# Kernel optimization log

Hardware: AMD Instinct MI355X
Metric: run time of the kernel (lower is better)

Reference implementation:

```python
import jax, jax.numpy as jnp
import numpy as np

D_MODEL = 1024
D_STATE = 16
D_CONV = 4
EXPAND = 2
D_INNER = EXPAND * D_MODEL
B, L = 4, 2048


def setup_inputs() -> dict:
    key = jax.random.key(0)
    ks = jax.random.split(key, 8)
    s = 0.02
    x = jax.random.normal(ks[0], (B, L, D_MODEL), jnp.float32)
    W_in = jax.random.normal(ks[1], (D_MODEL, 2 * D_INNER), jnp.float32) * s
    conv_w = jax.random.normal(ks[2], (D_INNER, D_CONV), jnp.float32) * 0.1
    conv_b = jnp.zeros((D_INNER,), jnp.float32)
    W_x = jax.random.normal(ks[3], (D_INNER, 1 + 2 * D_STATE), jnp.float32) * s
    w_dt = jax.random.normal(ks[4], (D_INNER,), jnp.float32) * 0.1
    b_dt = jnp.zeros((D_INNER,), jnp.float32)
    # A_log initialized exactly as in the torch module: log of [1..d_state] per channel
    A_log = jnp.log(jnp.tile(jnp.arange(1, D_STATE + 1, dtype=jnp.float32), (D_INNER, 1)))
    D = jnp.ones((D_INNER,), jnp.float32)
    W_out = jax.random.normal(ks[5], (D_INNER, D_MODEL), jnp.float32) * s
    return {"x": x, "W_in": W_in, "conv_w": conv_w, "conv_b": conv_b,
            "W_x": W_x, "w_dt": w_dt, "b_dt": b_dt, "A_log": A_log,
            "D": D, "W_out": W_out}


def _mamba_forward(x, W_in, conv_w, conv_b, W_x, w_dt, b_dt, A_log, D, W_out):
    Bb, Ll, _ = x.shape
    # input projection -> x branch and gate z
    xz = x @ W_in                                  # [B, L, 2*d_inner]
    xc, z = jnp.split(xz, 2, axis=-1)
    # depthwise causal conv1d (left-pad d_conv-1, cross-correlation like torch Conv1d)
    xp = jnp.pad(xc, ((0, 0), (D_CONV - 1, 0), (0, 0)))
    xconv = conv_b
    for k in range(D_CONV):                        # tiny fixed kernel loop
        xconv = xconv + xp[:, k:k + Ll, :] * conv_w[:, k]
    xs = jax.nn.silu(xconv)                        # [B, L, d_inner]
    # selective SSM parameters
    A = -jnp.exp(A_log)                            # [d_inner, d_state]
    x_dbl = xs @ W_x                               # [B, L, 1+2N]
    d_raw = x_dbl[..., :1]
    Bp = x_dbl[..., 1:1 + D_STATE]                 # [B, L, N]
    Cp = x_dbl[..., 1 + D_STATE:]                  # [B, L, N]
    delta = jax.nn.softplus(d_raw * w_dt + b_dt)   # [B, L, d_inner]

    def step(h, inp):
        dt, b, c, xt = inp                         # [B,d_inner],[B,N],[B,N],[B,d_inner]
        At = jnp.exp(dt[..., None] * A)            # [B, d_inner, N]
        h = At * h + (dt * xt)[..., None] * b[:, None, :]
        y = jnp.einsum('bdn,bn->bd', h, c)
        return h, y

    h0 = jnp.zeros((Bb, D_INNER, D_STATE), x.dtype)
    seq = (jnp.swapaxes(delta, 0, 1), jnp.swapaxes(Bp, 0, 1),
           jnp.swapaxes(Cp, 0, 1), jnp.swapaxes(xs, 0, 1))
    _, ys = jax.lax.scan(step, h0, seq)            # ys: [L, B, d_inner]
    y = jnp.swapaxes(ys, 0, 1) + xs * D
    y = y * jax.nn.silu(z)
    return y @ W_out                               # [B, L, d_model]


def reference(x, W_in, conv_w, conv_b, W_x, w_dt, b_dt, A_log, D, W_out):
    return _mamba_forward(x, W_in, conv_w, conv_b, W_x, w_dt, b_dt, A_log, D, W_out)
```

## Files before the change

### kernel.cpp

```cpp
#include <hip/hip_runtime.h>
#include <hip/hip_bf16.h>


typedef __attribute__((ext_vector_type(8))) short short8;
typedef __attribute__((ext_vector_type(8))) __bf16 bf16x8;
typedef __attribute__((ext_vector_type(4))) float f32x4;

__device__ inline short bf16_bits(float f) {
  __hip_bfloat16 h = __float2bfloat16(f);
  return *(short*)&h;
}

__global__ void transpose_cast_kernel(const float* __restrict__ in,
                                      __hip_bfloat16* __restrict__ out, int R, int C) {
  __shared__ float tile[32][33];
  int tx = threadIdx.x, ty = threadIdx.y;
  int x = blockIdx.x * 32 + tx;
  int y0 = blockIdx.y * 32;
#pragma unroll
  for (int j = 0; j < 32; j += 8)
    tile[ty + j][tx] = in[(size_t)(y0 + ty + j) * C + x];
  __syncthreads();
  int x2 = y0 + tx;
  int y2 = blockIdx.x * 32;
#pragma unroll
  for (int j = 0; j < 32; j += 8)
    out[(size_t)(y2 + ty + j) * R + x2] = __float2bfloat16(tile[tx][ty + j]);
}

__global__ void wx_pad_kernel(const float* __restrict__ wx,
                              __hip_bfloat16* __restrict__ out) {
  int i = blockIdx.x * 256 + threadIdx.x;
  int j = i >> 11;
  int k = i & 2047;
  float v = (j < 33) ? wx[k * 33 + j] : 0.f;
  out[i] = __float2bfloat16(v);
}

__global__ __launch_bounds__(256) void gemm_bt(
    const void* __restrict__ Aptr, const __hip_bfloat16* __restrict__ BTbf,
    void* __restrict__ C0, void* __restrict__ C1,
    int M, int N, int K, int a_f32, int mode) {
  __shared__ __align__(16) short As[128 * 32];
  __shared__ __align__(16) short Bs[128 * 32];
  int tid = threadIdx.x;
  int bm = blockIdx.y, bn = blockIdx.x;
  int lane = tid & 63, w = tid >> 6;
  int wm = w >> 1, wn = w & 1;
  int l16 = lane & 15, quad = lane >> 4;

  int Kslice = K / (int)gridDim.z;
  int kbeg = (int)blockIdx.z * Kslice;

  f32x4 acc[4][4] = {};

  const short* Ag16 = (const short*)Aptr + (size_t)bm * 128 * K + kbeg;
  const float* Ag32 = (const float*)Aptr + (size_t)bm * 128 * K + kbeg;
  const short* Bg = (const short*)BTbf + (size_t)bn * 128 * K + kbeg;

  int r0 = tid >> 2;
  int c0 = (tid & 3) * 8;

  for (int k0 = 0; k0 < Kslice; k0 += 32) {
    short8 a0, a1;
    if (a_f32) {
      const float* p0 = &Ag32[(size_t)r0 * K + k0 + c0];
      const float* p1 = &Ag32[(size_t)(r0 + 64) * K + k0 + c0];
      float4 u0 = *(const float4*)p0, v0 = *(const float4*)(p0 + 4);
      float4 u1 = *(const float4*)p1, v1 = *(const float4*)(p1 + 4);
      a0[0] = bf16_bits(u0.x); a0[1] = bf16_bits(u0.y);
      a0[2] = bf16_bits(u0.z); a0[3] = bf16_bits(u0.w);
      a0[4] = bf16_bits(v0.x); a0[5] = bf16_bits(v0.y);
      a0[6] = bf16_bits(v0.z); a0[7] = bf16_bits(v0.w);
      a1[0] = bf16_bits(u1.x); a1[1] = bf16_bits(u1.y);
      a1[2] = bf16_bits(u1.z); a1[3] = bf16_bits(u1.w);
      a1[4] = bf16_bits(v1.x); a1[5] = bf16_bits(v1.y);
      a1[6] = bf16_bits(v1.z); a1[7] = bf16_bits(v1.w);
    } else {
      a0 = *(const short8*)&Ag16[(size_t)r0 * K + k0 + c0];
      a1 = *(const short8*)&Ag16[(size_t)(r0 + 64) * K + k0 + c0];
    }
    short8 b0 = *(const short8*)&Bg[(size_t)r0 * K + k0 + c0];
    short8 b1 = *(const short8*)&Bg[(size_t)(r0 + 64) * K + k0 + c0];
    __syncthreads();
    *(short8*)&As[r0 * 32 + c0] = a0;
    *(short8*)&As[(r0 + 64) * 32 + c0] = a1;
    *(short8*)&Bs[r0 * 32 + c0] = b0;
    *(short8*)&Bs[(r0 + 64) * 32 + c0] = b1;
    __syncthreads();

    bf16x8 af[4], bfr[4];
#pragma unroll
    for (int mt = 0; mt < 4; ++mt)
      af[mt] = *(bf16x8*)&As[(wm * 64 + mt * 16 + l16) * 32 + quad * 8];
#pragma unroll
    for (int nt = 0; nt < 4; ++nt)
      bfr[nt] = *(bf16x8*)&Bs[(wn * 64 + nt * 16 + l16) * 32 + quad * 8];
#pragma unroll
    for (int mt = 0; mt < 4; ++mt)
#pragma unroll
      for (int nt = 0; nt < 4; ++nt)
        acc[mt][nt] = __builtin_amdgcn_mfma_f32_16x16x32_bf16(af[mt], bfr[nt],
                                                              acc[mt][nt], 0, 0, 0);
  }

#pragma unroll
  for (int mt = 0; mt < 4; ++mt) {
#pragma unroll
    for (int nt = 0; nt < 4; ++nt) {
#pragma unroll
      for (int i = 0; i < 4; ++i) {
        int row = bm * 128 + wm * 64 + mt * 16 + quad * 4 + i;
        int col = bn * 128 + wn * 64 + nt * 16 + l16;
        float v = acc[mt][nt][i];
        if (mode == 0) {
          ((float*)C0)[(size_t)row * N + col] = v;
        } else if (mode == 2) {
          atomicAdd(&((float*)C0)[(size_t)row * N + col], v);
        } else {
          if (col < 2048) {
            ((__hip_bfloat16*)C0)[(size_t)row * 2048 + col] = __float2bfloat16(v);
          } else {
            float s = v / (1.f + __expf(-v));
            ((__hip_bfloat16*)C1)[(size_t)row * 2048 + (col - 2048)] =
                __float2bfloat16(s);
          }
        }
      }
    }
  }
}

__global__ void conv_silu_kernel(const __hip_bfloat16* __restrict__ xc,
                                 const float* __restrict__ conv_w,
                                 const float* __restrict__ conv_b,
                                 __hip_bfloat16* __restrict__ xs_bf) {
  int i = blockIdx.x * 256 + threadIdx.x;
  int d = i & 2047;
  int row = i >> 11;
  int l = row & 2047;
  float acc = conv_b[d];
#pragma unroll
  for (int k = 0; k < 4; ++k) {
    int lj = l - 3 + k;
    if (lj >= 0)
      acc += __bfloat162float(xc[(size_t)(row - 3 + k) * 2048 + d]) * conv_w[d * 4 + k];
  }
  float s = acc / (1.f + __expf(-acc));
  xs_bf[i] = __float2bfloat16(s);
}

template <int FINAL>
__global__ __launch_bounds__(256) void scan_seg(
    const float* __restrict__ xdbl, const __hip_bfloat16* __restrict__ xs,
    const __hip_bfloat16* __restrict__ sz,
    const float* __restrict__ w_dt, const float* __restrict__ b_dt,
    const float* __restrict__ Dvec, const float* __restrict__ hio,
    float* __restrict__ hloc, float* __restrict__ sdtA,
    __hip_bfloat16* __restrict__ y_bf) {
  const int t = threadIdx.x;
  const int b = blockIdx.y, seg = blockIdx.z;
  const int d = blockIdx.x * 256 + t;
  const int brow0 = b * 2048 + seg * 128;

  __shared__ __align__(16) float s_xd[16][36];
  __shared__ ushort s_xs[16][256];
  __shared__ ushort s_sz[16][256];

  float h[16];
  const float wdt = w_dt[d], bdt = b_dt[d];
  float Dd = 0.f, sdt = 0.f;
  const size_t hbase = ((size_t)(seg * 4 + b) * 2048 + d) * 16;
  if (FINAL) {
    Dd = Dvec[d];
#pragma unroll
    for (int n = 0; n < 16; n += 4) *(float4*)&h[n] = *(const float4*)&hio[hbase + n];
  } else {
#pragma unroll
    for (int n = 0; n < 16; ++n) h[n] = 0.f;
  }

  for (int c = 0; c < 8; ++c) {
    const int r0 = brow0 + c * 16;
    __syncthreads();
    if (t < 144) {
      int row = t / 9, q = t - row * 9;
      *(float4*)&s_xd[row][q * 4] =
          *(const float4*)&xdbl[(size_t)(r0 + row) * 128 + q * 4];
    }
#pragma unroll
    for (int r = 0; r < 16; ++r) {
      s_xs[r][t] = ((const ushort*)xs)[(size_t)(r0 + r) * 2048 + d];
      if (FINAL) s_sz[r][t] = ((const ushort*)sz)[(size_t)(r0 + r) * 2048 + d];
    }
    __syncthreads();
#pragma unroll
    for (int r = 0; r < 16; ++r) {
      float pre = __builtin_fmaf(s_xd[r][0], wdt, bdt);
      float ex = __expf(pre);
      float dtv = (pre > 20.f) ? pre : __logf(1.f + ex);
      float E = __expf(-dtv);
      float p2 = E * E, p4 = p2 * p2, p8 = p4 * p4;
      float at[16];
      at[0] = E;        at[1] = p2;       at[2] = p2 * E;   at[3] = p4;
      at[4] = p4 * E;   at[5] = p4 * p2;  at[6] = p4 * at[2]; at[7] = p8;
      at[8] = p8 * E;   at[9] = p8 * p2;  at[10] = p8 * at[2]; at[11] = p8 * p4;
      at[12] = p8 * at[4]; at[13] = p8 * at[5]; at[14] = p8 * at[6]; at[15] = p8 * p8;
      ushort ux = s_xs[r][t];
      float xsv = __bfloat162float(*(__hip_bfloat16*)&ux);
      float w = dtv * xsv;
      float y = 0.f;
#pragma unroll
      for (int n = 0; n < 16; ++n) {
        h[n] = __builtin_fmaf(at[n], h[n], w * s_xd[r][1 + n]);
        if (FINAL) y = __builtin_fmaf(h[n], s_xd[r][17 + n], y);
      }
      if (FINAL) {
        ushort uz = s_sz[r][t];
        float szv = __bfloat162float(*(__hip_bfloat16*)&uz);
        float yv = (y + xsv * Dd) * szv;
        y_bf[(size_t)(r0 + r) * 2048 + d] = __float2bfloat16(yv);
      } else {
        sdt += dtv;
      }
    }
  }
  if (!FINAL) {
#pragma unroll
    for (int n = 0; n < 16; n += 4) *(float4*)&hloc[hbase + n] = *(const float4*)&h[n];
    sdtA[(seg * 4 + b) * 2048 + d] = sdt;
  }
}

__global__ void scan_mid(float* __restrict__ hio, const float* __restrict__ sdtA,
                         const float* __restrict__ A_log) {
  int gid = blockIdx.x * 256 + threadIdx.x;
  int n = gid & 15, dd = (gid >> 4) & 2047;
  float A = -__expf(A_log[dd * 16 + n]);
  float h = 0.f;
#pragma unroll
  for (int s = 0; s < 16; ++s) {
    float v = hio[s * 131072 + gid];
    float P = __expf(A * sdtA[s * 8192 + (gid >> 4)]);
    float nh = __builtin_fmaf(P, h, v);
    hio[s * 131072 + gid] = h;
    h = nh;
  }
}

extern "C" void kernel_launch(void* const* d_in, const int* in_sizes, int n_in,
                              void* d_out, int out_size, void* d_ws, size_t ws_size,
                              hipStream_t stream) {
  const float* x      = (const float*)d_in[0];
  const float* W_in   = (const float*)d_in[1];
  const float* conv_w = (const float*)d_in[2];
  const float* conv_b = (const float*)d_in[3];
  const float* W_x    = (const float*)d_in[4];
  const float* w_dt   = (const float*)d_in[5];
  const float* b_dt   = (const float*)d_in[6];
  const float* A_log  = (const float*)d_in[7];
  const float* Dv     = (const float*)d_in[8];
  const float* W_out  = (const float*)d_in[9];
  float* out = (float*)d_out;

  char* ws = (char*)d_ws;
  const size_t MB = 1ull << 20;
  __hip_bfloat16* xc_bf = (__hip_bfloat16*)(ws + 0);
  __hip_bfloat16* y_bf  = (__hip_bfloat16*)(ws + 0);
  __hip_bfloat16* sz_bf = (__hip_bfloat16*)(ws + 32 * MB);
  __hip_bfloat16* xs_bf = (__hip_bfloat16*)(ws + 64 * MB);
  __hip_bfloat16* WinT  = (__hip_bfloat16*)(ws + 96 * MB);
  float*          hio   = (float*)(ws + 96 * MB);
  __hip_bfloat16* WoutT = (__hip_bfloat16*)(ws + 104 * MB);
  __hip_bfloat16* WxT   = (__hip_bfloat16*)(ws + 108 * MB);
  float*          sdtA  = (float*)(ws + 108 * MB);
  float*          xdbl  = (float*)(ws + 108 * MB + 512 * 1024);

  transpose_cast_kernel<<<dim3(128, 32), dim3(32, 8), 0, stream>>>(W_in, WinT, 1024, 4096);
  transpose_cast_kernel<<<dim3(32, 64), dim3(32, 8), 0, stream>>>(W_out, WoutT, 2048, 1024);
  wx_pad_kernel<<<1024, 256, 0, stream>>>(W_x, WxT);

  gemm_bt<<<dim3(32, 64), 256, 0, stream>>>(x, WinT, xc_bf, sz_bf, 8192, 4096, 1024, 1, 1);
  conv_silu_kernel<<<65536, 256, 0, stream>>>(xc_bf, conv_w, conv_b, xs_bf);
  hipMemsetAsync(xdbl, 0, 8192 * 128 * sizeof(float), stream);
  gemm_bt<<<dim3(1, 64, 4), 256, 0, stream>>>(xs_bf, WxT, xdbl, nullptr, 8192, 128, 2048, 0, 2);

  scan_seg<0><<<dim3(8, 4, 16), 256, 0, stream>>>(xdbl, xs_bf, nullptr, w_dt, b_dt,
                                                  nullptr, nullptr, hio, sdtA, nullptr);
  scan_mid<<<512, 256, 0, stream>>>(hio, sdtA, A_log);
  scan_seg<1><<<dim3(8, 4, 16), 256, 0, stream>>>(xdbl, xs_bf, sz_bf, w_dt, b_dt,
                                                  Dv, hio, nullptr, nullptr, y_bf);

  gemm_bt<<<dim3(8, 64), 256, 0, stream>>>(y_bf, WoutT, out, nullptr, 8192, 1024, 2048, 0, 0);
}
```

Before: 517.0 us.

## Use direct global-to-LDS loads in GEMM, pre-cast x, vectorize conv

```diff
diff --git a/kernel.cpp b/kernel.cpp
--- a/kernel.cpp
+++ b/kernel.cpp
@@ -5,10 +5,32 @@
 typedef __attribute__((ext_vector_type(8))) short short8;
 typedef __attribute__((ext_vector_type(8))) __bf16 bf16x8;
 typedef __attribute__((ext_vector_type(4))) float f32x4;
+typedef __attribute__((ext_vector_type(8))) unsigned short ushort8v;
+typedef __attribute__((ext_vector_type(4))) unsigned short ushort4v;
 
 __device__ inline short bf16_bits(float f) {
   __hip_bfloat16 h = __float2bfloat16(f);
   return *(short*)&h;
+}
+__device__ inline float bfbits2f(unsigned short u) {
+  return __uint_as_float(((unsigned)u) << 16);
+}
+
+#define GLL16(gp, lp)                                                        \
+  __builtin_amdgcn_global_load_lds(                                          \
+      (const __attribute__((address_space(1))) void*)(gp),                   \
+      (__attribute__((address_space(3))) void*)(lp), 16, 0, 0)
+
+__global__ void cast_bf16_kernel(const float* __restrict__ in,
+                                 unsigned short* __restrict__ out) {
+  int i = blockIdx.x * 256 + threadIdx.x;
+  float4 v = ((const float4*)in)[i];
+  ushort4v o;
+  o.x = (unsigned short)bf16_bits(v.x);
+  o.y = (unsigned short)bf16_bits(v.y);
+  o.z = (unsigned short)bf16_bits(v.z);
+  o.w = (unsigned short)bf16_bits(v.w);
+  *(ushort4v*)&out[4 * i] = o;
 }
 
 __global__ void transpose_cast_kernel(const float* __restrict__ in,
@@ -38,9 +60,9 @@
 }
 
 __global__ __launch_bounds__(256) void gemm_bt(
-    const void* __restrict__ Aptr, const __hip_bfloat16* __restrict__ BTbf,
+    const __hip_bfloat16* __restrict__ Abf, const __hip_bfloat16* __restrict__ BTbf,
     void* __restrict__ C0, void* __restrict__ C1,
-    int M, int N, int K, int a_f32, int mode) {
+    int M, int N, int K, int mode) {
   __shared__ __align__(16) short As[128 * 32];
   __shared__ __align__(16) short Bs[128 * 32];
   int tid = threadIdx.x;
@@ -54,39 +76,22 @@
 
   f32x4 acc[4][4] = {};
 
-  const short* Ag16 = (const short*)Aptr + (size_t)bm * 128 * K + kbeg;
-  const float* Ag32 = (const float*)Aptr + (size_t)bm * 128 * K + kbeg;
+  const short* Ag = (const short*)Abf + (size_t)bm * 128 * K + kbeg;
   const short* Bg = (const short*)BTbf + (size_t)bn * 128 * K + kbeg;
 
-  int r0 = tid >> 2;
-  int c0 = (tid & 3) * 8;
+  int srow = w * 16 + (lane >> 2);
+  int scol = (lane & 3) * 8;
+  const short* agp = &Ag[(size_t)srow * K + scol];
+  const short* bgp = &Bg[(size_t)srow * K + scol];
+  short* asl = &As[w * 512];
+  short* bsl = &Bs[w * 512];
 
   for (int k0 = 0; k0 < Kslice; k0 += 32) {
-    short8 a0, a1;
-    if (a_f32) {
-      const float* p0 = &Ag32[(size_t)r0 * K + k0 + c0];
-      const float* p1 = &Ag32[(size_t)(r0 + 64) * K + k0 + c0];
-      float4 u0 = *(const float4*)p0, v0 = *(const float4*)(p0 + 4);
-      float4 u1 = *(const float4*)p1, v1 = *(const float4*)(p1 + 4);
-      a0[0] = bf16_bits(u0.x); a0[1] = bf16_bits(u0.y);
-      a0[2] = bf16_bits(u0.z); a0[3] = bf16_bits(u0.w);
-      a0[4] = bf16_bits(v0.x); a0[5] = bf16_bits(v0.y);
-      a0[6] = bf16_bits(v0.z); a0[7] = bf16_bits(v0.w);
-      a1[0] = bf16_bits(u1.x); a1[1] = bf16_bits(u1.y);
-      a1[2] = bf16_bits(u1.z); a1[3] = bf16_bits(u1.w);
-      a1[4] = bf16_bits(v1.x); a1[5] = bf16_bits(v1.y);
-      a1[6] = bf16_bits(v1.z); a1[7] = bf16_bits(v1.w);
-    } else {
-      a0 = *(const short8*)&Ag16[(size_t)r0 * K + k0 + c0];
-      a1 = *(const short8*)&Ag16[(size_t)(r0 + 64) * K + k0 + c0];
-    }
-    short8 b0 = *(const short8*)&Bg[(size_t)r0 * K + k0 + c0];
-    short8 b1 = *(const short8*)&Bg[(size_t)(r0 + 64) * K + k0 + c0];
     __syncthreads();
-    *(short8*)&As[r0 * 32 + c0] = a0;
-    *(short8*)&As[(r0 + 64) * 32 + c0] = a1;
-    *(short8*)&Bs[r0 * 32 + c0] = b0;
-    *(short8*)&Bs[(r0 + 64) * 32 + c0] = b1;
+    GLL16(agp + k0, asl);
+    GLL16(agp + (size_t)64 * K + k0, asl + 64 * 32);
+    GLL16(bgp + k0, bsl);
+    GLL16(bgp + (size_t)64 * K + k0, bsl + 64 * 32);
     __syncthreads();
 
     bf16x8 af[4], bfr[4];
@@ -131,23 +136,44 @@
   }
 }
 
-__global__ void conv_silu_kernel(const __hip_bfloat16* __restrict__ xc,
+__global__ void conv_silu_kernel(const unsigned short* __restrict__ xc,
                                  const float* __restrict__ conv_w,
                                  const float* __restrict__ conv_b,
-                                 __hip_bfloat16* __restrict__ xs_bf) {
+                                 unsigned short* __restrict__ xs_bf) {
   int i = blockIdx.x * 256 + threadIdx.x;
-  int d = i & 2047;
-  int row = i >> 11;
+  int g = i & 255;
+  int row = i >> 8;
   int l = row & 2047;
-  float acc = conv_b[d];
+  int d = g * 8;
+
+  float4 cw[8];
+#pragma unroll
+  for (int j = 0; j < 8; ++j) cw[j] = ((const float4*)conv_w)[d + j];
+
+  float acc[8];
+  {
+    float4 b0 = ((const float4*)conv_b)[g * 2];
+    float4 b1 = ((const float4*)conv_b)[g * 2 + 1];
+    acc[0] = b0.x; acc[1] = b0.y; acc[2] = b0.z; acc[3] = b0.w;
+    acc[4] = b1.x; acc[5] = b1.y; acc[6] = b1.z; acc[7] = b1.w;
+  }
 #pragma unroll
   for (int k = 0; k < 4; ++k) {
-    int lj = l - 3 + k;
-    if (lj >= 0)
-      acc += __bfloat162float(xc[(size_t)(row - 3 + k) * 2048 + d]) * conv_w[d * 4 + k];
-  }
-  float s = acc / (1.f + __expf(-acc));
-  xs_bf[i] = __float2bfloat16(s);
+    if (l - 3 + k >= 0) {
+      ushort8v v = *(const ushort8v*)&xc[(size_t)(row - 3 + k) * 2048 + d];
+      const float* wk = (const float*)cw;
+#pragma unroll
+      for (int j = 0; j < 8; ++j)
+        acc[j] = __builtin_fmaf(bfbits2f(v[j]), wk[j * 4 + k], acc[j]);
+    }
+  }
+  ushort8v o;
+#pragma unroll
+  for (int j = 0; j < 8; ++j) {
+    float s = acc[j] / (1.f + __expf(-acc[j]));
+    o[j] = (unsigned short)bf16_bits(s);
+  }
+  *(ushort8v*)&xs_bf[(size_t)row * 2048 + d] = o;
 }
 
 template <int FINAL>
@@ -202,12 +228,11 @@
       float E = __expf(-dtv);
       float p2 = E * E, p4 = p2 * p2, p8 = p4 * p4;
       float at[16];
-      at[0] = E;        at[1] = p2;       at[2] = p2 * E;   at[3] = p4;
+      at[0] = E;        at[1] = p2;       at[2] = p2 * E;     at[3] = p4;
       at[4] = p4 * E;   at[5] = p4 * p2;  at[6] = p4 * at[2]; at[7] = p8;
       at[8] = p8 * E;   at[9] = p8 * p2;  at[10] = p8 * at[2]; at[11] = p8 * p4;
       at[12] = p8 * at[4]; at[13] = p8 * at[5]; at[14] = p8 * at[6]; at[15] = p8 * p8;
-      ushort ux = s_xs[r][t];
-      float xsv = __bfloat162float(*(__hip_bfloat16*)&ux);
+      float xsv = bfbits2f(s_xs[r][t]);
       float w = dtv * xsv;
       float y = 0.f;
 #pragma unroll
@@ -216,8 +241,7 @@
         if (FINAL) y = __builtin_fmaf(h[n], s_xd[r][17 + n], y);
       }
       if (FINAL) {
-        ushort uz = s_sz[r][t];
-        float szv = __bfloat162float(*(__hip_bfloat16*)&uz);
+        float szv = bfbits2f(s_sz[r][t]);
         float yv = (y + xsv * Dd) * szv;
         y_bf[(size_t)(r0 + r) * 2048 + d] = __float2bfloat16(yv);
       } else {
@@ -269,6 +293,7 @@
   __hip_bfloat16* y_bf  = (__hip_bfloat16*)(ws + 0);
   __hip_bfloat16* sz_bf = (__hip_bfloat16*)(ws + 32 * MB);
   __hip_bfloat16* xs_bf = (__hip_bfloat16*)(ws + 64 * MB);
+  __hip_bfloat16* x_bf  = (__hip_bfloat16*)(ws + 64 * MB);
   __hip_bfloat16* WinT  = (__hip_bfloat16*)(ws + 96 * MB);
   float*          hio   = (float*)(ws + 96 * MB);
   __hip_bfloat16* WoutT = (__hip_bfloat16*)(ws + 104 * MB);
@@ -276,14 +301,16 @@
   float*          sdtA  = (float*)(ws + 108 * MB);
   float*          xdbl  = (float*)(ws + 108 * MB + 512 * 1024);
 
+  cast_bf16_kernel<<<8192, 256, 0, stream>>>(x, (unsigned short*)x_bf);
   transpose_cast_kernel<<<dim3(128, 32), dim3(32, 8), 0, stream>>>(W_in, WinT, 1024, 4096);
   transpose_cast_kernel<<<dim3(32, 64), dim3(32, 8), 0, stream>>>(W_out, WoutT, 2048, 1024);
   wx_pad_kernel<<<1024, 256, 0, stream>>>(W_x, WxT);
 
-  gemm_bt<<<dim3(32, 64), 256, 0, stream>>>(x, WinT, xc_bf, sz_bf, 8192, 4096, 1024, 1, 1);
-  conv_silu_kernel<<<65536, 256, 0, stream>>>(xc_bf, conv_w, conv_b, xs_bf);
+  gemm_bt<<<dim3(32, 64), 256, 0, stream>>>(x_bf, WinT, xc_bf, sz_bf, 8192, 4096, 1024, 1);
+  conv_silu_kernel<<<8192, 256, 0, stream>>>((const unsigned short*)xc_bf, conv_w, conv_b,
+                                             (unsigned short*)xs_bf);
   hipMemsetAsync(xdbl, 0, 8192 * 128 * sizeof(float), stream);
-  gemm_bt<<<dim3(1, 64, 4), 256, 0, stream>>>(xs_bf, WxT, xdbl, nullptr, 8192, 128, 2048, 0, 2);
+  gemm_bt<<<dim3(1, 64, 4), 256, 0, stream>>>(xs_bf, WxT, xdbl, nullptr, 8192, 128, 2048, 2);
 
   scan_seg<0><<<dim3(8, 4, 16), 256, 0, stream>>>(xdbl, xs_bf, nullptr, w_dt, b_dt,
                                                   nullptr, nullptr, hio, sdtA, nullptr);
@@ -291,5 +318,5 @@
   scan_seg<1><<<dim3(8, 4, 16), 256, 0, stream>>>(xdbl, xs_bf, sz_bf, w_dt, b_dt,
                                                   Dv, hio, nullptr, nullptr, y_bf);
 
-  gemm_bt<<<dim3(8, 64), 256, 0, stream>>>(y_bf, WoutT, out, nullptr, 8192, 1024, 2048, 0, 0);
-}
+  gemm_bt<<<dim3(8, 64), 256, 0, stream>>>(y_bf, WoutT, out, nullptr, 8192, 1024, 2048, 0);
+}
```

After: 493.6 us. -4.5%, faster.
